# Optimization experiments

Measured on AMD Instinct MI355X. Metric: run time of the kernel, lower is better.

## Reference

```python
import jax, jax.numpy as jnp
import numpy as np


def setup_inputs() -> dict:
    key = jax.random.key(0)
    ka, kb = jax.random.split(key)
    B, S, I, J = 8, 8192, 256, 256
    a = jax.random.normal(ka, (B, S, I), dtype=jnp.float32)
    b = jax.random.normal(kb, (B, S, J), dtype=jnp.float32)
    return {"a": a, "b": b}


def reference(a, b):
    # mean_s(a_si outer b_sj) == (a^T @ b) / s, without materializing [*, i, j, s]
    s = a.shape[-2]
    out = jnp.einsum('...si,...sj->...ij', a, b) / s  # [*, i, j]
    return out
```

## Files before the change

### kernel.cpp

```cpp
#include <hip/hip_runtime.h>

typedef __bf16 bf16x8 __attribute__((ext_vector_type(8)));
typedef float f32x16 __attribute__((ext_vector_type(16)));
typedef float f32x4 __attribute__((ext_vector_type(4)));

#define S_TOTAL 8192
#define DIM 256
#define BK 16
#define NSP 16

__global__ __launch_bounds__(512, 6) void opm_partial(
    const float* __restrict__ A, const float* __restrict__ Bm,
    __bf16* __restrict__ dstbf, float* __restrict__ dstf32,
    int nsp, int kc, float scale)
{
    __shared__ float lA[2][BK * 256];
    __shared__ float lB[2][BK * 64];

    const int tid = threadIdx.x;
    const int w   = tid >> 6;
    const int l   = tid & 63;

    const int bid = blockIdx.x;
    const int x   = bid & 7;
    const int s   = bid >> 3;
    const int jq  = s & 3;
    const int gx  = s >> 2;
    const int g   = gx * 8 + x;
    const int batch = g / nsp;
    const int sp    = g % nsp;

    const long long base = (long long)batch * S_TOTAL * DIM;
    const int s0 = sp * kc;
    const int wr = w >> 1, wc = w & 1;
    const int lane31 = l & 31;
    const int hi = l >> 5;
    const int niter = kc / BK;

    f32x16 acc[2] = {};

    auto issue = [&](int it) {
        const int b2 = it & 1;
        const long long sb = (long long)(s0 + it * BK);
        __builtin_amdgcn_global_load_lds(
            (const __attribute__((address_space(1))) unsigned int*)(A + base + (sb + w) * DIM + 4 * l),
            (__attribute__((address_space(3))) unsigned int*)&lA[b2][w * 256], 16, 0, 0);
        __builtin_amdgcn_global_load_lds(
            (const __attribute__((address_space(1))) unsigned int*)(A + base + (sb + w + 8) * DIM + 4 * l),
            (__attribute__((address_space(3))) unsigned int*)&lA[b2][(w + 8) * 256], 16, 0, 0);
        if (w < 4) {
            __builtin_amdgcn_global_load_lds(
                (const __attribute__((address_space(1))) unsigned int*)(Bm + base + (sb + 4 * w + (l >> 4)) * DIM + jq * 64 + 4 * (l & 15)),
                (__attribute__((address_space(3))) unsigned int*)&lB[b2][4 * w * 64], 16, 0, 0);
        }
    };

    auto compute = [&](int b2) {
        const int i0 = wr * 64 + lane31;
        const int j0 = wc * 32 + lane31;
        bf16x8 af[2], bfv;
        #pragma unroll
        for (int mi = 0; mi < 2; ++mi)
            #pragma unroll
            for (int e = 0; e < 8; ++e)
                af[mi][e] = (__bf16)lA[b2][(hi * 8 + e) * 256 + i0 + mi * 32];
        #pragma unroll
        for (int e = 0; e < 8; ++e)
            bfv[e] = (__bf16)lB[b2][(hi * 8 + e) * 64 + j0];
        acc[0] = __builtin_amdgcn_mfma_f32_32x32x16_bf16(af[0], bfv, acc[0], 0, 0, 0);
        acc[1] = __builtin_amdgcn_mfma_f32_32x32x16_bf16(af[1], bfv, acc[1], 0, 0, 0);
    };

    issue(0);
    issue(1);

    for (int it = 0; it < niter; ++it) {
        if (it == 0) {
            if (w < 4) asm volatile("s_waitcnt vmcnt(3)" ::: "memory");
            else       asm volatile("s_waitcnt vmcnt(2)" ::: "memory");
        } else {
            asm volatile("s_waitcnt vmcnt(0)" ::: "memory");
        }
        __builtin_amdgcn_s_barrier();
        if (it >= 1 && it + 1 < niter) issue(it + 1);
        compute(it & 1);
    }

    if (dstf32) {
        float* o = dstf32 + (long long)batch * (256 * 256) + jq * 64;
        #pragma unroll
        for (int mi = 0; mi < 2; ++mi)
        #pragma unroll
        for (int q = 0; q < 16; ++q) {
            const int row = (q & 3) + 8 * (q >> 2) + 4 * hi;
            const int i = wr * 64 + mi * 32 + row;
            const int j = wc * 32 + lane31;
            o[i * 256 + j] = acc[mi][q] * scale;
        }
    } else {
        __bf16* o = dstbf + (long long)((batch * nsp + sp) * 4 + jq) * 16384;
        __bf16* ebuf = (__bf16*)&lA[0][0];
        #pragma unroll
        for (int band = 0; band < 2; ++band) {
            __syncthreads();
            if ((wr >> 1) == band) {
                #pragma unroll
                for (int mi = 0; mi < 2; ++mi)
                #pragma unroll
                for (int q = 0; q < 16; ++q) {
                    const int lr = (wr & 1) * 64 + mi * 32 + (q & 3) + 8 * (q >> 2) + 4 * hi;
                    ebuf[lr * 64 + wc * 32 + lane31] = (__bf16)(acc[mi][q] * scale);
                }
            }
            __syncthreads();
            #pragma unroll
            for (int h = 0; h < 2; ++h) {
                const int G = tid + h * 512;
                *(bf16x8*)&o[band * 8192 + G * 8] = *(const bf16x8*)&ebuf[G * 8];
            }
        }
    }
}

__global__ __launch_bounds__(256) void opm_reduce16(
    const __bf16* __restrict__ ws, float* __restrict__ out)
{
    const int idx = blockIdx.x * 256 + threadIdx.x;
    const int batch = idx >> 13;
    const int gg  = idx & 8191;
    const int i   = gg >> 5;
    const int jgc = gg & 31;
    const int jq  = jgc >> 3;
    const int c8  = (jgc & 7) * 8;

    const bf16x8* p = (const bf16x8*)(ws + ((long long)(batch * NSP) * 4 + jq) * 16384 + i * 64 + c8);
    bf16x8 v[NSP];
    #pragma unroll
    for (int sp = 0; sp < NSP; ++sp) v[sp] = p[sp * 8192];

    float sacc[8] = {0.f, 0.f, 0.f, 0.f, 0.f, 0.f, 0.f, 0.f};
    #pragma unroll
    for (int sp = 0; sp < NSP; ++sp)
        #pragma unroll
        for (int e = 0; e < 8; ++e) sacc[e] += (float)v[sp][e];

    f32x4 lo = { sacc[0], sacc[1], sacc[2], sacc[3] };
    f32x4 hiv = { sacc[4], sacc[5], sacc[6], sacc[7] };
    lo  *= (1.0f / 8192.0f);
    hiv *= (1.0f / 8192.0f);
    ((f32x4*)out)[idx * 2]     = lo;
    ((f32x4*)out)[idx * 2 + 1] = hiv;
}

extern "C" void kernel_launch(void* const* d_in, const int* in_sizes, int n_in,
                              void* d_out, int out_size, void* d_ws, size_t ws_size,
                              hipStream_t stream)
{
    (void)in_sizes; (void)n_in; (void)out_size;
    const float* A  = (const float*)d_in[0];
    const float* Bm = (const float*)d_in[1];
    float* out = (float*)d_out;

    if (ws_size >= (size_t)8 * NSP * 4 * 16384 * sizeof(__bf16)) {
        opm_partial<<<32 * NSP, 512, 0, stream>>>(A, Bm, (__bf16*)d_ws, nullptr,
                                                  NSP, S_TOTAL / NSP, 1.0f);
        opm_reduce16<<<256, 256, 0, stream>>>((const __bf16*)d_ws, out);
    } else {
        opm_partial<<<32, 512, 0, stream>>>(A, Bm, nullptr, out, 1, S_TOTAL, 1.0f / 8192.0f);
    }
}
```

Baseline: 39.69 us.

## Split output tiles into 128x64 blocks and double the S-split count

Each workgroup now computes a 128x64 tile (half of i) with 256 threads instead of a 256x64 tile with 512 threads. The S dimension is split into 32 chunks instead of 16, giving 2048 workgroups and a 32-way bf16 reduction. The intent is more parallelism and smaller LDS use per block for better occupancy and latency hiding. In exchange, the A chunks loaded per block carry no reuse across the i-halves, so each B row is read twice, and the partial workspace plus reduction traffic doubles.

```diff
diff --git a/kernel.cpp b/kernel.cpp
--- a/kernel.cpp
+++ b/kernel.cpp
@@ -7,26 +7,28 @@
 #define S_TOTAL 8192
 #define DIM 256
 #define BK 16
-#define NSP 16
+#define NSP 32
 
-__global__ __launch_bounds__(512, 6) void opm_partial(
+__global__ __launch_bounds__(256, 6) void opm_partial(
     const float* __restrict__ A, const float* __restrict__ Bm,
     __bf16* __restrict__ dstbf, float* __restrict__ dstf32,
     int nsp, int kc, float scale)
 {
-    __shared__ float lA[2][BK * 256];
+    __shared__ float lA[2][BK * 128];
     __shared__ float lB[2][BK * 64];
 
     const int tid = threadIdx.x;
     const int w   = tid >> 6;
     const int l   = tid & 63;
 
-    const int bid = blockIdx.x;
-    const int x   = bid & 7;
-    const int s   = bid >> 3;
-    const int jq  = s & 3;
-    const int gx  = s >> 2;
-    const int g   = gx * 8 + x;
+    const int bid  = blockIdx.x;
+    const int x    = bid & 7;
+    const int r    = bid >> 3;
+    const int mate = r & 7;
+    const int gx   = r >> 3;
+    const int jq   = mate >> 1;
+    const int ih   = mate & 1;
+    const int g    = gx * 8 + x;
     const int batch = g / nsp;
     const int sp    = g % nsp;
 
@@ -42,31 +44,29 @@
     auto issue = [&](int it) {
         const int b2 = it & 1;
         const long long sb = (long long)(s0 + it * BK);
+        #pragma unroll
+        for (int q = 0; q < 2; ++q) {
+            __builtin_amdgcn_global_load_lds(
+                (const __attribute__((address_space(1))) unsigned int*)(
+                    A + base + (sb + 4 * w + 2 * q + (l >> 5)) * DIM + ih * 128 + 4 * (l & 31)),
+                (__attribute__((address_space(3))) unsigned int*)&lA[b2][(4 * w + 2 * q) * 128], 16, 0, 0);
+        }
         __builtin_amdgcn_global_load_lds(
-            (const __attribute__((address_space(1))) unsigned int*)(A + base + (sb + w) * DIM + 4 * l),
-            (__attribute__((address_space(3))) unsigned int*)&lA[b2][w * 256], 16, 0, 0);
-        __builtin_amdgcn_global_load_lds(
-            (const __attribute__((address_space(1))) unsigned int*)(A + base + (sb + w + 8) * DIM + 4 * l),
-            (__attribute__((address_space(3))) unsigned int*)&lA[b2][(w + 8) * 256], 16, 0, 0);
-        if (w < 4) {
-            __builtin_amdgcn_global_load_lds(
-                (const __attribute__((address_space(1))) unsigned int*)(Bm + base + (sb + 4 * w + (l >> 4)) * DIM + jq * 64 + 4 * (l & 15)),
-                (__attribute__((address_space(3))) unsigned int*)&lB[b2][4 * w * 64], 16, 0, 0);
-        }
+            (const __attribute__((address_space(1))) unsigned int*)(
+                Bm + base + (sb + 4 * w + (l >> 4)) * DIM + jq * 64 + 4 * (l & 15)),
+            (__attribute__((address_space(3))) unsigned int*)&lB[b2][4 * w * 64], 16, 0, 0);
     };
 
     auto compute = [&](int b2) {
-        const int i0 = wr * 64 + lane31;
-        const int j0 = wc * 32 + lane31;
         bf16x8 af[2], bfv;
         #pragma unroll
         for (int mi = 0; mi < 2; ++mi)
             #pragma unroll
             for (int e = 0; e < 8; ++e)
-                af[mi][e] = (__bf16)lA[b2][(hi * 8 + e) * 256 + i0 + mi * 32];
+                af[mi][e] = (__bf16)lA[b2][(hi * 8 + e) * 128 + wr * 64 + mi * 32 + lane31];
         #pragma unroll
         for (int e = 0; e < 8; ++e)
-            bfv[e] = (__bf16)lB[b2][(hi * 8 + e) * 64 + j0];
+            bfv[e] = (__bf16)lB[b2][(hi * 8 + e) * 64 + wc * 32 + lane31];
         acc[0] = __builtin_amdgcn_mfma_f32_32x32x16_bf16(af[0], bfv, acc[0], 0, 0, 0);
         acc[1] = __builtin_amdgcn_mfma_f32_32x32x16_bf16(af[1], bfv, acc[1], 0, 0, 0);
     };
@@ -75,65 +75,57 @@
     issue(1);
 
     for (int it = 0; it < niter; ++it) {
-        if (it == 0) {
-            if (w < 4) asm volatile("s_waitcnt vmcnt(3)" ::: "memory");
-            else       asm volatile("s_waitcnt vmcnt(2)" ::: "memory");
-        } else {
-            asm volatile("s_waitcnt vmcnt(0)" ::: "memory");
-        }
+        if (it == 0) asm volatile("s_waitcnt vmcnt(3)" ::: "memory");
+        else         asm volatile("s_waitcnt vmcnt(0)" ::: "memory");
         __builtin_amdgcn_s_barrier();
         if (it >= 1 && it + 1 < niter) issue(it + 1);
         compute(it & 1);
     }
 
     if (dstf32) {
-        float* o = dstf32 + (long long)batch * (256 * 256) + jq * 64;
+        float* o = dstf32 + (long long)batch * (256 * 256) + ih * 128 * 256 + jq * 64;
         #pragma unroll
         for (int mi = 0; mi < 2; ++mi)
         #pragma unroll
         for (int q = 0; q < 16; ++q) {
             const int row = (q & 3) + 8 * (q >> 2) + 4 * hi;
-            const int i = wr * 64 + mi * 32 + row;
-            const int j = wc * 32 + lane31;
-            o[i * 256 + j] = acc[mi][q] * scale;
+            o[(wr * 64 + mi * 32 + row) * 256 + wc * 32 + lane31] = acc[mi][q] * scale;
         }
     } else {
-        __bf16* o = dstbf + (long long)((batch * nsp + sp) * 4 + jq) * 16384;
+        __bf16* o = dstbf + (long long)((batch * nsp + sp) * 8 + mate) * 8192;
         __bf16* ebuf = (__bf16*)&lA[0][0];
+        __syncthreads();
         #pragma unroll
-        for (int band = 0; band < 2; ++band) {
-            __syncthreads();
-            if ((wr >> 1) == band) {
-                #pragma unroll
-                for (int mi = 0; mi < 2; ++mi)
-                #pragma unroll
-                for (int q = 0; q < 16; ++q) {
-                    const int lr = (wr & 1) * 64 + mi * 32 + (q & 3) + 8 * (q >> 2) + 4 * hi;
-                    ebuf[lr * 64 + wc * 32 + lane31] = (__bf16)(acc[mi][q] * scale);
-                }
-            }
-            __syncthreads();
-            #pragma unroll
-            for (int h = 0; h < 2; ++h) {
-                const int G = tid + h * 512;
-                *(bf16x8*)&o[band * 8192 + G * 8] = *(const bf16x8*)&ebuf[G * 8];
-            }
+        for (int mi = 0; mi < 2; ++mi)
+        #pragma unroll
+        for (int q = 0; q < 16; ++q) {
+            const int row = wr * 64 + mi * 32 + (q & 3) + 8 * (q >> 2) + 4 * hi;
+            ebuf[row * 64 + wc * 32 + lane31] = (__bf16)(acc[mi][q] * scale);
+        }
+        __syncthreads();
+        #pragma unroll
+        for (int h = 0; h < 4; ++h) {
+            const int G = tid + h * 256;
+            *(bf16x8*)&o[G * 8] = *(const bf16x8*)&ebuf[G * 8];
         }
     }
 }
 
-__global__ __launch_bounds__(256) void opm_reduce16(
+__global__ __launch_bounds__(256) void opm_reduce32(
     const __bf16* __restrict__ ws, float* __restrict__ out)
 {
     const int idx = blockIdx.x * 256 + threadIdx.x;
     const int batch = idx >> 13;
     const int gg  = idx & 8191;
     const int i   = gg >> 5;
-    const int jgc = gg & 31;
-    const int jq  = jgc >> 3;
-    const int c8  = (jgc & 7) * 8;
+    const int jc  = gg & 31;
+    const int jq  = jc >> 3;
+    const int ihh = i >> 7;
+    const int ir  = i & 127;
+    const int c8  = (jc & 7) * 8;
 
-    const bf16x8* p = (const bf16x8*)(ws + ((long long)(batch * NSP) * 4 + jq) * 16384 + i * 64 + c8);
+    const bf16x8* p = (const bf16x8*)(ws
+        + ((long long)(batch * NSP) * 8 + jq * 2 + ihh) * 8192 + ir * 64 + c8);
     bf16x8 v[NSP];
     #pragma unroll
     for (int sp = 0; sp < NSP; ++sp) v[sp] = p[sp * 8192];
@@ -161,11 +153,11 @@
     const float* Bm = (const float*)d_in[1];
     float* out = (float*)d_out;
 
-    if (ws_size >= (size_t)8 * NSP * 4 * 16384 * sizeof(__bf16)) {
-        opm_partial<<<32 * NSP, 512, 0, stream>>>(A, Bm, (__bf16*)d_ws, nullptr,
-                                                  NSP, S_TOTAL / NSP, 1.0f);
-        opm_reduce16<<<256, 256, 0, stream>>>((const __bf16*)d_ws, out);
+    if (ws_size >= (size_t)8 * NSP * 8 * 8192 * sizeof(__bf16)) {
+        opm_partial<<<8 * NSP * 8, 256, 0, stream>>>(A, Bm, (__bf16*)d_ws, nullptr,
+                                                     NSP, S_TOTAL / NSP, 1.0f);
+        opm_reduce32<<<256, 256, 0, stream>>>((const __bf16*)d_ws, out);
     } else {
-        opm_partial<<<32, 512, 0, stream>>>(A, Bm, nullptr, out, 1, S_TOTAL, 1.0f / 8192.0f);
+        opm_partial<<<64, 256, 0, stream>>>(A, Bm, nullptr, out, 1, S_TOTAL, 1.0f / 8192.0f);
     }
 }
```

Measured after the change: 43.21 us. 1.09x slower.
